# Kernel optimization log

Hardware: AMD Instinct MI355X
Metric: run time of the kernel (lower is better)

Reference implementation:

```python
import jax, jax.numpy as jnp
import numpy as np

B, N = 16384, 31
N_INTS, N_OPS, N_PASSES = 10, 4, 4
NODE_LIT, NODE_OP = 0, 1


def setup_inputs() -> dict:
    key = jax.random.key(0)
    ks = jax.random.split(key, 7)
    cats = jax.random.randint(ks[0], (B, N), 0, 2)
    ops = jax.random.randint(ks[1], (B, N), 0, N_OPS)
    lits = jax.random.randint(ks[2], (B, N), 0, N_INTS)
    left = jax.random.randint(ks[3], (B, N), 0, N)
    right = jax.random.randint(ks[4], (B, N), 0, N)
    mask = jnp.ones((B, N), dtype=bool)
    op_table = jax.random.normal(ks[5], (N_OPS, N_INTS, N_INTS, N_INTS), dtype=jnp.float32) * 0.1
    return {"cats": cats, "ops": ops, "lits": lits, "left": left,
            "right": right, "mask": mask, "op_table": op_table}


def reference(cats, ops, lits, left, right, mask, op_table):
    left = jnp.clip(left, 0, N - 1)
    right = jnp.clip(right, 0, N - 1)
    ops_c = jnp.clip(ops, 0, N_OPS - 1)

    # init: literals -> one-hot over ints, everything else zero
    lit_mask = (cats == NODE_LIT) & mask                     # (B, N)
    lit_onehot = jax.nn.one_hot(jnp.clip(lits, 0, N_INTS - 1), N_INTS, dtype=jnp.float32)
    state = jnp.where(lit_mask[..., None], lit_onehot, 0.0)  # (B, N, n_ints)

    op_mask = (cats == NODE_OP) & mask
    brow = jnp.arange(B)[:, None]
    slice_table = op_table[ops_c]                             # (B, N, i, j, k)

    def op_step(state):
        left_dist = state[brow, left]                         # (B, N, n_ints)
        right_dist = state[brow, right]                       # (B, N, n_ints)
        logits = jnp.einsum('bni,bnj,bnijk->bnk', left_dist, right_dist, slice_table)
        dist = jax.nn.softmax(logits, axis=-1)
        new_state = jnp.where(op_mask[..., None], dist, state)
        return new_state, logits

    for _ in range(N_PASSES - 1):
        state, _ = op_step(state)
    state, node_logits = op_step(state)

    root_is_lit = (cats[:, 0] == NODE_LIT)[:, None].astype(jnp.float32)
    lit_logits = state[:, 0, :] * 10.0
    root_logits = root_is_lit * lit_logits + (1.0 - root_is_lit) * node_logits[:, 0, :]
    return root_logits
```

## Files before the change

### kernel.cpp

```cpp
#include <hip/hip_runtime.h>

#define NB 16384
#define NN 31
#define NI 10
#define NOPS 4
#define GB 32
#define TPB 512
#define NWAVES 8
#define NPB (GB * NN)
#define NDR_TOT 672
#define INVALID_NODE 0xFFFFu

typedef __attribute__((ext_vector_type(8))) short bf16x8_t;
typedef __attribute__((ext_vector_type(4))) float f32x4_t;

template <int CTRL>
__device__ __forceinline__ float dppf(float v) {
    return __int_as_float(__builtin_amdgcn_update_dpp(
        0, __float_as_int(v), CTRL, 0xF, 0xF, true));
}
__device__ __forceinline__ float rowsum16(float x) {
    x += dppf<0xB1>(x);
    x += dppf<0x4E>(x);
    x += dppf<0x124>(x);
    x += dppf<0x128>(x);
    return x;
}
__device__ __forceinline__ unsigned short f2bf(float f) {
    unsigned u = __float_as_uint(f);
    u += 0x7FFFu + ((u >> 16) & 1u);
    return (unsigned short)(u >> 16);
}
__device__ __forceinline__ unsigned cvtpk(float lo, float hi) {
    unsigned r;
    asm("v_cvt_pk_bf16_f32 %0, %1, %2" : "=v"(r) : "v"(lo), "v"(hi));
    return r;
}
__device__ __forceinline__ int ndrOff(int p) {
    return (p == 0) ? 0 : (p == 1) ? 304 : (p == 2) ? 480 : 592;
}

__global__ __launch_bounds__(TPB, 4) void listops_mfma(
    const int* __restrict__ cats, const int* __restrict__ ops,
    const int* __restrict__ lits, const int* __restrict__ left,
    const int* __restrict__ right, const float* __restrict__ tbl,
    float* __restrict__ out)
{
    __shared__ __align__(16) float st[NPB][12];
    __shared__ __align__(16) unsigned short Bl[NOPS * 4 * 64 * 8];
    __shared__ unsigned chLR[NPB];
    __shared__ unsigned short chIdx[NPB];
    __shared__ unsigned opm[GB];
    __shared__ unsigned short ndr[NDR_TOT];
    __shared__ int cntA[16], cntB[16], baseA[16], ntP[4];
    __shared__ unsigned char tOpA[4][20];

    const int tid = threadIdx.x;
    const int wv  = tid >> 6;
    const int l   = tid & 63;
    const int q   = l >> 4;
    const int c   = l & 15;

    float* tscr = &st[0][0];
    if (tid < 16) { cntA[tid] = 0; cntB[tid] = 0; }
    if (tid < GB) opm[tid] = 0u;
    ndr[tid] = (unsigned short)INVALID_NODE;
    if (tid < NDR_TOT - TPB) ndr[TPB + tid] = (unsigned short)INVALID_NODE;
    {
        const float4* ts = (const float4*)tbl;
        float4* td = (float4*)tscr;
        if (tid < 1000) {
            td[tid] = ts[tid];
            if (tid < 488) td[tid + 512] = ts[tid + 512];
        }
    }
    __syncthreads();

    #pragma unroll
    for (int rr = 0; rr < 2; ++rr) {
        const int fi   = tid + rr * TPB;
        const int lane = fi & 63;
        const int step = (fi >> 6) & 3;
        const int op   = fi >> 8;
        const int bq = lane >> 4, bn = lane & 15;
        unsigned short v[8];
        #pragma unroll
        for (int e = 0; e < 8; ++e) {
            float val = 0.0f;
            if (bn < NI) {
                if (step < 2) {
                    val = tscr[((op * NI + 4 * step + bq) * NI + e) * NI + bn];
                } else if (step == 2) {
                    if (bq < 2) val = tscr[((op * NI + 8 + bq) * NI + e) * NI + bn];
                } else {
                    if (bq < 2)      val = tscr[((op * NI + e) * NI + 8 + bq) * NI + bn];
                    else if (e < 2)  val = tscr[((op * NI + 8 + e) * NI + 8 + (bq - 2)) * NI + bn];
                }
            }
            v[e] = f2bf(val);
        }
        uint4 pk;
        pk.x = (unsigned)v[0] | ((unsigned)v[1] << 16);
        pk.y = (unsigned)v[2] | ((unsigned)v[3] << 16);
        pk.z = (unsigned)v[4] | ((unsigned)v[5] << 16);
        pk.w = (unsigned)v[6] | ((unsigned)v[7] << 16);
        ((uint4*)&Bl[0])[fi] = pk;
    }
    __syncthreads();

    #pragma unroll
    for (int rr = 0; rr < 2; ++rr) {
        int n = tid + rr * TPB;
        if (n < NPB) {
            int g   = blockIdx.x * NPB + n;
            int cat = cats[g];
            int op  = min(max(ops[g], 0), NOPS - 1);
            int lit = min(max(lits[g], 0), NI - 1);
            int b   = n / NN;
            int nl  = n - b * NN;
            int cl  = min(max(left[g],  0), NN - 1);
            int cr  = min(max(right[g], 0), NN - 1);
            chLR[n]  = (unsigned)((b * NN + cl) * 48)
                     | ((unsigned)((b * NN + cr) * 48) << 16);
            chIdx[n] = (unsigned short)(cl | (cr << 5) | (op << 10));
            float4* rp = (float4*)&st[n][0];
            rp[0] = make_float4(0.f, 0.f, 0.f, 0.f);
            rp[1] = make_float4(0.f, 0.f, 0.f, 0.f);
            rp[2] = make_float4(0.f, 0.f, 0.f, 0.f);
            if (cat == 0) {
                st[n][lit] = 1.0f;
                if (nl == 0) {
                    float* o = out + (blockIdx.x * GB + b) * NI;
                    #pragma unroll
                    for (int k = 0; k < NI; ++k) o[k] = (k == lit) ? 10.0f : 0.0f;
                }
            } else {
                atomicOr(&opm[b], 1u << nl);
            }
        }
    }
    __syncthreads();

    unsigned M0 = 0, M1 = 0, M2 = 0, M3 = 0;
    if (tid < GB) {
        const int b = tid;
        const unsigned om = opm[b];
        M3 = om & 1u;
        unsigned m = M3, F;
        F = 0;
        while (m) { int n = __builtin_ctz(m); m &= m - 1;
            unsigned ch = chIdx[b * NN + n];
            F |= (1u << (ch & 31)) | (1u << ((ch >> 5) & 31)); }
        M2 = F & om;
        m = M2; F = 0;
        while (m) { int n = __builtin_ctz(m); m &= m - 1;
            unsigned ch = chIdx[b * NN + n];
            F |= (1u << (ch & 31)) | (1u << ((ch >> 5) & 31)); }
        M1 = F & om;
        m = M1; F = 0;
        while (m) { int n = __builtin_ctz(m); m &= m - 1;
            unsigned ch = chIdx[b * NN + n];
            F |= (1u << (ch & 31)) | (1u << ((ch >> 5) & 31)); }
        M0 = F & om;
        #pragma unroll
        for (int p = 0; p < 4; ++p) {
            unsigned mm = (p == 0) ? M0 : (p == 1) ? M1 : (p == 2) ? M2 : M3;
            while (mm) {
                int n = __builtin_ctz(mm); mm &= mm - 1;
                int o = (chIdx[b * NN + n] >> 10) & 3;
                atomicAdd(&cntA[p * 4 + o], 1);
            }
        }
    }
    __syncthreads();
    if (tid == 0) {
        #pragma unroll
        for (int p = 0; p < 4; ++p) {
            int rb = 0, tc = 0;
            #pragma unroll
            for (int o = 0; o < NOPS; ++o) {
                baseA[p * 4 + o] = rb;
                int nt = (cntA[p * 4 + o] + 15) >> 4;
                for (int i = 0; i < nt; ++i) tOpA[p][tc++] = (unsigned char)o;
                rb += nt << 4;
            }
            ntP[p] = tc;
        }
    }
    __syncthreads();
    if (tid < GB) {
        const int b = tid;
        #pragma unroll
        for (int p = 0; p < 4; ++p) {
            unsigned mm = (p == 0) ? M0 : (p == 1) ? M1 : (p == 2) ? M2 : M3;
            const int off = ndrOff(p);
            while (mm) {
                int n = __builtin_ctz(mm); mm &= mm - 1;
                int o = (chIdx[b * NN + n] >> 10) & 3;
                int r = atomicAdd(&cntB[p * 4 + o], 1);
                ndr[off + baseA[p * 4 + o] + r] = (unsigned short)((b << 5) | n);
            }
        }
    }
    __syncthreads();

    const char* sb = (const char*)&st[0][0];
    #pragma unroll 1
    for (int pass = 0; pass < 4; ++pass) {
        const unsigned short* nd = &ndr[ndrOff(pass)];
        const unsigned char* top = &tOpA[pass][0];
        const int nt = ntP[pass];
        f32x4_t acc[3];

        #pragma unroll
        for (int i = 0; i < 3; ++i) {
            int t = wv + NWAVES * i;
            if (t < nt) {
                int rowv = nd[t * 16 + c];
                int idx  = (rowv == (int)INVALID_NODE) ? 0
                         : ((rowv >> 5) * NN + (rowv & 31));
                unsigned lrp = chLR[idx];
                const char* Lb = sb + (lrp & 0xFFFFu);
                const char* Rb = sb + (lrp >> 16);
                float4 l0  = *(const float4*)Lb;
                float4 l1  = *(const float4*)(Lb + 16);
                float2 l89 = *(const float2*)(Lb + 32);
                float4 r0  = *(const float4*)Rb;
                float4 r1  = *(const float4*)(Rb + 16);
                float2 r89 = *(const float2*)(Rb + 32);

                float lq0 = (q & 2) ? ((q & 1) ? l0.w : l0.z) : ((q & 1) ? l0.y : l0.x);
                float lq1 = (q & 2) ? ((q & 1) ? l1.w : l1.z) : ((q & 1) ? l1.y : l1.x);
                float lq2 = (q == 0) ? l89.x : ((q == 1) ? l89.y : 0.0f);

                float Re[8] = {r0.x, r0.y, r0.z, r0.w, r1.x, r1.y, r1.z, r1.w};
                float Le[8] = {l0.x, l0.y, l0.z, l0.w, l1.x, l1.y, l1.z, l1.w};

                bf16x8_t av0, av1, av2, av3;
                unsigned* a0 = (unsigned*)&av0;
                unsigned* a1 = (unsigned*)&av1;
                unsigned* a2 = (unsigned*)&av2;
                unsigned* a3 = (unsigned*)&av3;
                float rsel = (q & 1) ? r89.y : r89.x;
                const bool qlo = (q < 2);
                float w3[8];
                w3[0] = (qlo ? Le[0] : l89.x) * rsel;
                w3[1] = (qlo ? Le[1] : l89.y) * rsel;
                #pragma unroll
                for (int e = 2; e < 8; ++e) w3[e] = (qlo ? Le[e] : 0.0f) * rsel;
                #pragma unroll
                for (int d = 0; d < 4; ++d) {
                    a0[d] = cvtpk(lq0 * Re[2 * d], lq0 * Re[2 * d + 1]);
                    a1[d] = cvtpk(lq1 * Re[2 * d], lq1 * Re[2 * d + 1]);
                    a2[d] = cvtpk(lq2 * Re[2 * d], lq2 * Re[2 * d + 1]);
                    a3[d] = cvtpk(w3[2 * d], w3[2 * d + 1]);
                }

                const char* Bp = (const char*)&Bl[0] + (int)top[t] * 4096 + l * 16;
                f32x4_t a = {0.0f, 0.0f, 0.0f, 0.0f};
                a = __builtin_amdgcn_mfma_f32_16x16x32_bf16(av0, *(const bf16x8_t*)(Bp + 0 * 1024), a, 0, 0, 0);
                a = __builtin_amdgcn_mfma_f32_16x16x32_bf16(av1, *(const bf16x8_t*)(Bp + 1 * 1024), a, 0, 0, 0);
                a = __builtin_amdgcn_mfma_f32_16x16x32_bf16(av2, *(const bf16x8_t*)(Bp + 2 * 1024), a, 0, 0, 0);
                a = __builtin_amdgcn_mfma_f32_16x16x32_bf16(av3, *(const bf16x8_t*)(Bp + 3 * 1024), a, 0, 0, 0);
                acc[i] = a;
            }
        }
        __syncthreads();

        if (pass < 3) {
            #pragma unroll
            for (int i = 0; i < 3; ++i) {
                int t = wv + NWAVES * i;
                if (t < nt) {
                    f32x4_t a = acc[i];
                    ushort4 nds = *(const ushort4*)&nd[t * 16 + 4 * q];
                    const unsigned short* np = (const unsigned short*)&nds;
                    #pragma unroll
                    for (int r = 0; r < 4; ++r) {
                        float ex = (c < NI) ? __expf(a[r]) : 0.0f;
                        float sd = rowsum16(ex);
                        float pv = ex * __builtin_amdgcn_rcpf(sd);
                        unsigned short ndv = np[r];
                        if (ndv != (unsigned short)INVALID_NODE && c < NI) {
                            int i2 = ((int)ndv >> 5) * NN + ((int)ndv & 31);
                            st[i2][c] = pv;
                        }
                    }
                }
            }
            __syncthreads();
        } else {
            #pragma unroll
            for (int i = 0; i < 3; ++i) {
                int t = wv + NWAVES * i;
                if (t < nt) {
                    f32x4_t a = acc[i];
                    ushort4 nds = *(const ushort4*)&nd[t * 16 + 4 * q];
                    const unsigned short* np = (const unsigned short*)&nds;
                    #pragma unroll
                    for (int r = 0; r < 4; ++r) {
                        unsigned short ndv = np[r];
                        if (ndv != (unsigned short)INVALID_NODE && c < NI) {
                            int b = (int)ndv >> 5;
                            out[(blockIdx.x * GB + b) * NI + c] = a[r];
                        }
                    }
                }
            }
        }
    }
}

extern "C" void kernel_launch(void* const* d_in, const int* in_sizes, int n_in,
                              void* d_out, int out_size, void* d_ws, size_t ws_size,
                              hipStream_t stream) {
    const int*   cats     = (const int*)  d_in[0];
    const int*   ops      = (const int*)  d_in[1];
    const int*   lits     = (const int*)  d_in[2];
    const int*   left     = (const int*)  d_in[3];
    const int*   right    = (const int*)  d_in[4];
    const float* op_table = (const float*)d_in[6];
    float*       out      = (float*)      d_out;

    hipLaunchKernelGGL(listops_mfma, dim3(NB / GB), dim3(TPB), 0, stream,
                       cats, ops, lits, left, right, op_table, out);
}
```

Measured before the change: 18.26 us.

## Double block size and parallelize frontier and bucket construction across threads

Each block now handles 64 batch rows with 1024 threads and 16 waves instead of 32 rows with 512 threads, which halves the block count and amortizes the per-block table load and bf16 repack over twice as many rows. The serial per-row loops that computed the pass frontiers and scattered nodes into op buckets are replaced by node-parallel passes using shared atomics, with a barrier per level. Child offsets are stored in 16-byte units so they fit in 16 bits at the larger block size. Risks are fewer resident blocks per CU because of the larger shared memory footprint, more barriers, and up to 3 MFMA tiles per wave across 16 waves, which may not cover every tile in the worst case.

```diff
diff --git a/kernel.cpp b/kernel.cpp
--- a/kernel.cpp
+++ b/kernel.cpp
@@ -4,11 +4,12 @@
 #define NN 31
 #define NI 10
 #define NOPS 4
-#define GB 32
-#define TPB 512
-#define NWAVES 8
+#define GB 64
+#define TPB 1024
+#define NWAVES 16
 #define NPB (GB * NN)
-#define NDR_TOT 672
+#define NDR_TOT 1200
+#define MAXT_PW 3
 #define INVALID_NODE 0xFFFFu
 
 typedef __attribute__((ext_vector_type(8))) short bf16x8_t;
@@ -37,7 +38,7 @@
     return r;
 }
 __device__ __forceinline__ int ndrOff(int p) {
-    return (p == 0) ? 0 : (p == 1) ? 304 : (p == 2) ? 480 : 592;
+    return (p == 0) ? 0 : (p == 1) ? 572 : (p == 2) ? 888 : 1076;
 }
 
 __global__ __launch_bounds__(TPB, 4) void listops_mfma(
@@ -51,9 +52,10 @@
     __shared__ unsigned chLR[NPB];
     __shared__ unsigned short chIdx[NPB];
     __shared__ unsigned opm[GB];
+    __shared__ unsigned Mfr[4][GB];
     __shared__ unsigned short ndr[NDR_TOT];
     __shared__ int cntA[16], cntB[16], baseA[16], ntP[4];
-    __shared__ unsigned char tOpA[4][20];
+    __shared__ unsigned char tOpA[4][36];
 
     const int tid = threadIdx.x;
     const int wv  = tid >> 6;
@@ -63,22 +65,14 @@
 
     float* tscr = &st[0][0];
     if (tid < 16) { cntA[tid] = 0; cntB[tid] = 0; }
-    if (tid < GB) opm[tid] = 0u;
+    if (tid < GB) { opm[tid] = 0u; Mfr[0][tid] = 0u; Mfr[1][tid] = 0u; Mfr[2][tid] = 0u; }
     ndr[tid] = (unsigned short)INVALID_NODE;
     if (tid < NDR_TOT - TPB) ndr[TPB + tid] = (unsigned short)INVALID_NODE;
+    if (tid < 1000) ((float4*)tscr)[tid] = ((const float4*)tbl)[tid];
+    __syncthreads();
+
     {
-        const float4* ts = (const float4*)tbl;
-        float4* td = (float4*)tscr;
-        if (tid < 1000) {
-            td[tid] = ts[tid];
-            if (tid < 488) td[tid + 512] = ts[tid + 512];
-        }
-    }
-    __syncthreads();
-
-    #pragma unroll
-    for (int rr = 0; rr < 2; ++rr) {
-        const int fi   = tid + rr * TPB;
+        const int fi   = tid;
         const int lane = fi & 63;
         const int step = (fi >> 6) & 3;
         const int op   = fi >> 8;
@@ -120,8 +114,8 @@
             int nl  = n - b * NN;
             int cl  = min(max(left[g],  0), NN - 1);
             int cr  = min(max(right[g], 0), NN - 1);
-            chLR[n]  = (unsigned)((b * NN + cl) * 48)
-                     | ((unsigned)((b * NN + cr) * 48) << 16);
+            chLR[n]  = (unsigned)((b * NN + cl) * 3)
+                     | ((unsigned)((b * NN + cr) * 3) << 16);
             chIdx[n] = (unsigned short)(cl | (cr << 5) | (op << 10));
             float4* rp = (float4*)&st[n][0];
             rp[0] = make_float4(0.f, 0.f, 0.f, 0.f);
@@ -141,34 +135,35 @@
     }
     __syncthreads();
 
-    unsigned M0 = 0, M1 = 0, M2 = 0, M3 = 0;
-    if (tid < GB) {
-        const int b = tid;
-        const unsigned om = opm[b];
-        M3 = om & 1u;
-        unsigned m = M3, F;
-        F = 0;
-        while (m) { int n = __builtin_ctz(m); m &= m - 1;
-            unsigned ch = chIdx[b * NN + n];
-            F |= (1u << (ch & 31)) | (1u << ((ch >> 5) & 31)); }
-        M2 = F & om;
-        m = M2; F = 0;
-        while (m) { int n = __builtin_ctz(m); m &= m - 1;
-            unsigned ch = chIdx[b * NN + n];
-            F |= (1u << (ch & 31)) | (1u << ((ch >> 5) & 31)); }
-        M1 = F & om;
-        m = M1; F = 0;
-        while (m) { int n = __builtin_ctz(m); m &= m - 1;
-            unsigned ch = chIdx[b * NN + n];
-            F |= (1u << (ch & 31)) | (1u << ((ch >> 5) & 31)); }
-        M0 = F & om;
+    if (tid < GB) Mfr[3][tid] = opm[tid] & 1u;
+    __syncthreads();
+    #pragma unroll
+    for (int p = 3; p >= 1; --p) {
         #pragma unroll
-        for (int p = 0; p < 4; ++p) {
-            unsigned mm = (p == 0) ? M0 : (p == 1) ? M1 : (p == 2) ? M2 : M3;
-            while (mm) {
-                int n = __builtin_ctz(mm); mm &= mm - 1;
-                int o = (chIdx[b * NN + n] >> 10) & 3;
-                atomicAdd(&cntA[p * 4 + o], 1);
+        for (int rr = 0; rr < 2; ++rr) {
+            int n = tid + rr * TPB;
+            if (n < NPB) {
+                int b  = n / NN;
+                int nl = n - b * NN;
+                if (((opm[b] >> nl) & 1u) && ((Mfr[p][b] >> nl) & 1u)) {
+                    unsigned ch = chIdx[n];
+                    atomicOr(&Mfr[p - 1][b], (1u << (ch & 31)) | (1u << ((ch >> 5) & 31)));
+                }
+            }
+        }
+        __syncthreads();
+    }
+    #pragma unroll
+    for (int rr = 0; rr < 2; ++rr) {
+        int n = tid + rr * TPB;
+        if (n < NPB) {
+            int b  = n / NN;
+            int nl = n - b * NN;
+            if ((opm[b] >> nl) & 1u) {
+                int o = (chIdx[n] >> 10) & 3;
+                #pragma unroll
+                for (int p = 0; p < 4; ++p)
+                    if ((Mfr[p][b] >> nl) & 1u) atomicAdd(&cntA[p * 4 + o], 1);
             }
         }
     }
@@ -188,17 +183,22 @@
         }
     }
     __syncthreads();
-    if (tid < GB) {
-        const int b = tid;
-        #pragma unroll
-        for (int p = 0; p < 4; ++p) {
-            unsigned mm = (p == 0) ? M0 : (p == 1) ? M1 : (p == 2) ? M2 : M3;
-            const int off = ndrOff(p);
-            while (mm) {
-                int n = __builtin_ctz(mm); mm &= mm - 1;
-                int o = (chIdx[b * NN + n] >> 10) & 3;
-                int r = atomicAdd(&cntB[p * 4 + o], 1);
-                ndr[off + baseA[p * 4 + o] + r] = (unsigned short)((b << 5) | n);
+    #pragma unroll
+    for (int rr = 0; rr < 2; ++rr) {
+        int n = tid + rr * TPB;
+        if (n < NPB) {
+            int b  = n / NN;
+            int nl = n - b * NN;
+            if ((opm[b] >> nl) & 1u) {
+                int o = (chIdx[n] >> 10) & 3;
+                #pragma unroll
+                for (int p = 0; p < 4; ++p) {
+                    if ((Mfr[p][b] >> nl) & 1u) {
+                        int r = atomicAdd(&cntB[p * 4 + o], 1);
+                        ndr[ndrOff(p) + baseA[p * 4 + o] + r] =
+                            (unsigned short)((b << 5) | nl);
+                    }
+                }
             }
         }
     }
@@ -210,18 +210,18 @@
         const unsigned short* nd = &ndr[ndrOff(pass)];
         const unsigned char* top = &tOpA[pass][0];
         const int nt = ntP[pass];
-        f32x4_t acc[3];
+        f32x4_t acc[MAXT_PW];
 
         #pragma unroll
-        for (int i = 0; i < 3; ++i) {
+        for (int i = 0; i < MAXT_PW; ++i) {
             int t = wv + NWAVES * i;
             if (t < nt) {
                 int rowv = nd[t * 16 + c];
                 int idx  = (rowv == (int)INVALID_NODE) ? 0
                          : ((rowv >> 5) * NN + (rowv & 31));
                 unsigned lrp = chLR[idx];
-                const char* Lb = sb + (lrp & 0xFFFFu);
-                const char* Rb = sb + (lrp >> 16);
+                const char* Lb = sb + ((lrp & 0xFFFFu) << 4);
+                const char* Rb = sb + ((lrp >> 16) << 4);
                 float4 l0  = *(const float4*)Lb;
                 float4 l1  = *(const float4*)(Lb + 16);
                 float2 l89 = *(const float2*)(Lb + 32);
@@ -269,7 +269,7 @@
 
         if (pass < 3) {
             #pragma unroll
-            for (int i = 0; i < 3; ++i) {
+            for (int i = 0; i < MAXT_PW; ++i) {
                 int t = wv + NWAVES * i;
                 if (t < nt) {
                     f32x4_t a = acc[i];
@@ -291,7 +291,7 @@
             __syncthreads();
         } else {
             #pragma unroll
-            for (int i = 0; i < 3; ++i) {
+            for (int i = 0; i < MAXT_PW; ++i) {
                 int t = wv + NWAVES * i;
                 if (t < nt) {
                     f32x4_t a = acc[i];
```

After: 17.51 us. -4.1%, faster.
